# Performance work log

Hardware: AMD Instinct MI355X
Metric: run time of the kernel (lower is better)

## Reference

```python
import jax, jax.numpy as jnp
import numpy as np

NUM_NODES = 50000
D_IN = 256
D_OUT = 256
N_QUERIES = 128
PER_GROUP = 256            # edges per query group in the last step (> max_edges)
E1 = N_QUERIES * PER_GROUP # 32768
E0 = 32768
RATIO = 0.2                # ratio_update


def setup_inputs() -> dict:
    key = jax.random.key(0)
    ks = jax.random.split(key, 10)
    d4 = 4 * D_IN
    rng = np.random.default_rng(0)
    # last-step edges: col0 = query idx (sorted, equal-size groups), col6 = src, col7 = dst
    edges1 = np.zeros((E1, 8), np.int64)
    edges1[:, 0] = np.repeat(np.arange(N_QUERIES), PER_GROUP)
    edges1[:, 6] = rng.integers(0, NUM_NODES, E1)
    edges1[:, 7] = rng.integers(0, NUM_NODES, E1)
    # earlier-step edges
    edges0 = np.zeros((E0, 8), np.int64)
    edges0[:, 0] = rng.integers(0, N_QUERIES, E0)
    edges0[:, 6] = rng.integers(0, NUM_NODES, E0)
    edges0[:, 7] = rng.integers(0, NUM_NODES, E0)
    return {
        "visited_node_score": jax.random.uniform(ks[0], (NUM_NODES,), jnp.float32),
        "visited_node_representation": jax.random.normal(ks[1], (NUM_NODES, D_IN), jnp.float32),
        "selected_edges0": jnp.asarray(edges0),
        "selected_edges1": jnp.asarray(edges1),
        "rel_emb0": jax.random.normal(ks[2], (E0, D_IN), jnp.float32),
        "rel_emb1": jax.random.normal(ks[3], (E1, D_IN), jnp.float32),
        "query_src_ts_emb": jax.random.normal(ks[4], (N_QUERIES, D_IN), jnp.float32),
        "query_rel_emb": jax.random.normal(ks[5], (N_QUERIES, D_IN), jnp.float32),
        "Wq": jax.random.normal(ks[6], (d4, d4), jnp.float32) * np.sqrt(2.0 / d4),
        "Wk": jax.random.normal(ks[7], (d4, d4), jnp.float32) * np.sqrt(2.0 / d4),
        "Wl": jax.random.normal(ks[8], (D_OUT, D_IN), jnp.float32) * np.sqrt(2.0 / (D_IN + D_OUT)),
        "bl": jnp.zeros((D_OUT,), jnp.float32),
        "max_edges": 64,
    }


def _att_score(edges, node_repr, rel, qst_tab, qr_tab, Wq, Wk):
    # G3: sum(Q(cat(vi,rel,qst,qr)) * K(cat(vj,rel,qst,qr)), -1) per edge
    q, src, dst = edges[:, 0], edges[:, 6], edges[:, 7]
    qst, qr = qst_tab[q], qr_tab[q]
    left = jnp.concatenate([node_repr[src], rel, qst, qr], axis=-1)   # [E, 4d]
    right = jnp.concatenate([node_repr[dst], rel, qst, qr], axis=-1)  # [E, 4d]
    return jnp.sum((left @ Wq.T) * (right @ Wk.T), axis=-1)          # [E]


def _seg_softmax(logits, seg, n):
    m = jax.ops.segment_max(logits, seg, num_segments=n)
    e = jnp.exp(logits - m[seg])
    s = jax.ops.segment_sum(e, seg, num_segments=n)
    return e / s[seg]


def _update_repr(edges, node_repr, w, ratio):
    # sparse mm: out[src] += (1-ratio)*w_e*repr[dst]; + identity for non-src rows, + ratio*repr for src rows
    src, dst = edges[:, 6], edges[:, 7]
    n = node_repr.shape[0]
    agg = jax.ops.segment_sum(((1.0 - ratio) * w)[:, None] * node_repr[dst], src, num_segments=n)
    is_src = jnp.zeros((n,), bool).at[src].set(True)
    diag = jnp.where(is_src, ratio, 1.0)
    return agg + diag[:, None] * node_repr


def reference(visited_node_score, visited_node_representation, selected_edges0,
              selected_edges1, rel_emb0, rel_emb1, query_src_ts_emb, query_rel_emb,
              Wq, Wk, Wl, bl, max_edges):
    n = visited_node_representation.shape[0]
    nq = query_src_ts_emb.shape[0]
    pg = selected_edges1.shape[0] // nq
    # attention on last step's edges
    logits = _att_score(selected_edges1, visited_node_representation, rel_emb1,
                        query_src_ts_emb, query_rel_emb, Wq, Wk)
    src1 = selected_edges1[:, 6]
    src_score = visited_node_score[src1]
    soft = _seg_softmax(logits, src1, n)
    target = soft * src_score
    # per-query-group top-k pruning (each group has pg > k edges)
    _, ti = jax.lax.top_k(target.reshape(nq, pg), max_edges)  # [nq, k]
    orig_indices = (ti + (jnp.arange(nq) * pg)[:, None]).reshape(-1)
    pruned_edges = selected_edges1[orig_indices]
    pruned_src_score = src_score[orig_indices]
    pruned_soft = soft[orig_indices]
    # sparse scatter-aggregation of scores onto dst (col 7)
    updated_node_score = jax.ops.segment_sum(pruned_soft * pruned_src_score,
                                             pruned_edges[:, 7], num_segments=n)
    node_repr = _update_repr(pruned_edges, visited_node_representation, pruned_soft, RATIO)
    # back-propagate representations through the earlier step
    tl = _att_score(selected_edges0, node_repr, rel_emb0, query_src_ts_emb, query_rel_emb, Wq, Wk)
    ts = _seg_softmax(tl, selected_edges0[:, 6], n)
    node_repr = _update_repr(selected_edges0, node_repr, ts, RATIO)
    # bypass_forward: LeakyReLU(Linear(.))
    node_repr = jax.nn.leaky_relu(node_repr @ Wl.T + bl)
    return (updated_node_score, node_repr, pruned_edges, orig_indices)
```

## Files before the change

### kernel.cpp

```cpp
#include <hip/hip_runtime.h>

#define NN 50000
#define D 256
#define NQ 128
#define PG 256
#define NE 32768
#define ME 64
#define BCAP 32
#define KDIM 256
#define NKT 8

typedef _Float16 f16;
typedef __attribute__((ext_vector_type(4))) _Float16 f16x4;
typedef __attribute__((ext_vector_type(8))) _Float16 f16x8;
typedef __attribute__((ext_vector_type(4))) float f32x4;

#define MFMA16(a,b,c) __builtin_amdgcn_mfma_f32_16x16x32_f16(a,b,c,0,0,0)

__device__ __forceinline__ unsigned fenc(float f){
  unsigned b = __float_as_uint(f);
  return (b & 0x80000000u) ? ~b : (b | 0x80000000u);
}
__device__ __forceinline__ float fdec(unsigned u){
  unsigned b = (u & 0x80000000u) ? (u & 0x7fffffffu) : ~u;
  return __uint_as_float(b);
}
__device__ __forceinline__ void split8(float4 a, float4 b, f16x8& h, f16x8& l){
  float v[8] = {a.x,a.y,a.z,a.w,b.x,b.y,b.z,b.w};
#pragma unroll
  for (int i=0;i<8;++i){
    _Float16 hh = (_Float16)v[i];
    h[i] = hh;
    l[i] = (_Float16)(v[i] - (float)hh);
  }
}

template<int EPI>
__global__ __launch_bounds__(256) void hgemm(const float* __restrict__ A,
                                             int Mrows,
                                             const f16* __restrict__ Bh, const f16* __restrict__ Bl,
                                             float* __restrict__ C, int ldc,
                                             const float* __restrict__ bias)
{
  __shared__ f16 AsH[128*40], AsL[128*40], BsH[128*40], BsL[128*40];
  const int tid = threadIdx.x;
  const int rb = blockIdx.x*128, cb = blockIdx.y*128;
  const int row = tid >> 1, ko = (tid & 1)*16;
  const bool aok = (rb + row) < Mrows;
  const int lane = tid & 63, wv = tid >> 6;
  const int qrw = (wv & 1)*64, qcw = (wv >> 1)*64;
  const int lm = lane & 15, qd = lane >> 4;

  const float* gA = A + (size_t)(rb+row)*KDIM + ko;
  const f16* gBh = Bh + (size_t)(cb+row)*KDIM + ko;
  const f16* gBl = Bl + (size_t)(cb+row)*KDIM + ko;

  float4 pa0=make_float4(0.f,0.f,0.f,0.f), pa1=pa0, pa2=pa0, pa3=pa0;
  f16x8 pbh0, pbh1, pbl0, pbl1;
  if (aok){ pa0 = *(const float4*)gA;     pa1 = *(const float4*)(gA+4);
            pa2 = *(const float4*)(gA+8); pa3 = *(const float4*)(gA+12); }
  pbh0 = *(const f16x8*)gBh; pbh1 = *(const f16x8*)(gBh+8);
  pbl0 = *(const f16x8*)gBl; pbl1 = *(const f16x8*)(gBl+8);

  f32x4 acc[4][4];
#pragma unroll
  for (int t=0;t<4;++t)
#pragma unroll
    for (int u=0;u<4;++u)
#pragma unroll
      for (int r=0;r<4;++r) acc[t][u][r] = 0.f;

  const int wbase = row*40 + ko;
  for (int kt = 0; kt < NKT; ++kt){
    __syncthreads();
    {
      f16x8 h0,h1,l0,l1;
      split8(pa0,pa1,h0,l0); split8(pa2,pa3,h1,l1);
      *(f16x8*)(AsH + wbase) = h0; *(f16x8*)(AsH + wbase + 8) = h1;
      *(f16x8*)(AsL + wbase) = l0; *(f16x8*)(AsL + wbase + 8) = l1;
      *(f16x8*)(BsH + wbase) = pbh0; *(f16x8*)(BsH + wbase + 8) = pbh1;
      *(f16x8*)(BsL + wbase) = pbl0; *(f16x8*)(BsL + wbase + 8) = pbl1;
    }
    __syncthreads();
    if (kt+1 < NKT){
      const int k0 = (kt+1)*32;
      if (aok){ pa0 = *(const float4*)(gA + k0);     pa1 = *(const float4*)(gA + k0 + 4);
                pa2 = *(const float4*)(gA + k0 + 8); pa3 = *(const float4*)(gA + k0 + 12); }
      pbh0 = *(const f16x8*)(gBh + k0); pbh1 = *(const f16x8*)(gBh + k0 + 8);
      pbl0 = *(const f16x8*)(gBl + k0); pbl1 = *(const f16x8*)(gBl + k0 + 8);
    }
    f16x8 fah[4], fal[4], fbh[4], fbl[4];
#pragma unroll
    for (int t=0;t<4;++t){
      int off = (qrw + t*16 + lm)*40 + qd*8;
      fah[t] = *(const f16x8*)(AsH + off);
      fal[t] = *(const f16x8*)(AsL + off);
    }
#pragma unroll
    for (int u=0;u<4;++u){
      int off = (qcw + u*16 + lm)*40 + qd*8;
      fbh[u] = *(const f16x8*)(BsH + off);
      fbl[u] = *(const f16x8*)(BsL + off);
    }
#pragma unroll
    for (int t=0;t<4;++t)
#pragma unroll
      for (int u=0;u<4;++u){
        acc[t][u] = MFMA16(fah[t], fbh[u], acc[t][u]);
        acc[t][u] = MFMA16(fah[t], fbl[u], acc[t][u]);
        acc[t][u] = MFMA16(fal[t], fbh[u], acc[t][u]);
      }
  }
#pragma unroll
  for (int t=0;t<4;++t){
#pragma unroll
    for (int u=0;u<4;++u){
      int col = cb + qcw + u*16 + lm;
      f32x4 v = acc[t][u];
#pragma unroll
      for (int r=0;r<4;++r){
        int rg = rb + qrw + t*16 + qd*4 + r;
        if (rg < Mrows){
          float x = v[r];
          if (EPI==1){ x += bias[col]; x = x > 0.f ? x : 0.01f*x; }
          C[(size_t)rg*ldc + col] = x;
        }
      }
    }
  }
}

__global__ __launch_bounds__(256) void hgemm_rel(const float* __restrict__ A,
                                                 const f16* __restrict__ Bh, const f16* __restrict__ Bl,
                                                 const int* __restrict__ edges,
                                                 const float* __restrict__ H,
                                                 const float* __restrict__ Rel,
                                                 float* __restrict__ logits)
{
  __shared__ f16 AsH[128*40], AsL[128*40], BsH[128*40], BsL[128*40];
  __shared__ int sIdx[128];
  const int tid = threadIdx.x;
  const int rb = blockIdx.x*128, cb = blockIdx.y*128;
  const int sec = blockIdx.y >> 1;
  const int row = tid >> 1, ko = (tid & 1)*16;
  const int lane = tid & 63, wv = tid >> 6;
  const int qrw = (wv & 1)*64, qcw = (wv >> 1)*64;
  const int lm = lane & 15, qd = lane >> 4;

  if (tid < 128){
    int e = rb + tid;
    sIdx[tid] = (sec==0) ? edges[(size_t)e*8+6] : (sec==1 ? edges[(size_t)e*8+7] : 0);
  }

  const float* gA = A + (size_t)(rb+row)*KDIM + ko;
  const f16* gBh = Bh + (size_t)(cb+row)*KDIM + ko;
  const f16* gBl = Bl + (size_t)(cb+row)*KDIM + ko;

  float4 pa0 = *(const float4*)gA,     pa1 = *(const float4*)(gA+4);
  float4 pa2 = *(const float4*)(gA+8), pa3 = *(const float4*)(gA+12);
  f16x8 pbh0 = *(const f16x8*)gBh, pbh1 = *(const f16x8*)(gBh+8);
  f16x8 pbl0 = *(const f16x8*)gBl, pbl1 = *(const f16x8*)(gBl+8);

  f32x4 acc[4][4];
#pragma unroll
  for (int t=0;t<4;++t)
#pragma unroll
    for (int u=0;u<4;++u)
#pragma unroll
      for (int r=0;r<4;++r) acc[t][u][r] = 0.f;

  const int wbase = row*40 + ko;
  for (int kt = 0; kt < NKT; ++kt){
    __syncthreads();
    {
      f16x8 h0,h1,l0,l1;
      split8(pa0,pa1,h0,l0); split8(pa2,pa3,h1,l1);
      *(f16x8*)(AsH + wbase) = h0; *(f16x8*)(AsH + wbase + 8) = h1;
      *(f16x8*)(AsL + wbase) = l0; *(f16x8*)(AsL + wbase + 8) = l1;
      *(f16x8*)(BsH + wbase) = pbh0; *(f16x8*)(BsH + wbase + 8) = pbh1;
      *(f16x8*)(BsL + wbase) = pbl0; *(f16x8*)(BsL + wbase + 8) = pbl1;
    }
    __syncthreads();
    if (kt+1 < NKT){
      const int k0 = (kt+1)*32;
      pa0 = *(const float4*)(gA + k0);     pa1 = *(const float4*)(gA + k0 + 4);
      pa2 = *(const float4*)(gA + k0 + 8); pa3 = *(const float4*)(gA + k0 + 12);
      pbh0 = *(const f16x8*)(gBh + k0); pbh1 = *(const f16x8*)(gBh + k0 + 8);
      pbl0 = *(const f16x8*)(gBl + k0); pbl1 = *(const f16x8*)(gBl + k0 + 8);
    }
    f16x8 fah[4], fal[4], fbh[4], fbl[4];
#pragma unroll
    for (int t=0;t<4;++t){
      int off = (qrw + t*16 + lm)*40 + qd*8;
      fah[t] = *(const f16x8*)(AsH + off);
      fal[t] = *(const f16x8*)(AsL + off);
    }
#pragma unroll
    for (int u=0;u<4;++u){
      int off = (qcw + u*16 + lm)*40 + qd*8;
      fbh[u] = *(const f16x8*)(BsH + off);
      fbl[u] = *(const f16x8*)(BsL + off);
    }
#pragma unroll
    for (int t=0;t<4;++t)
#pragma unroll
      for (int u=0;u<4;++u){
        acc[t][u] = MFMA16(fah[t], fbh[u], acc[t][u]);
        acc[t][u] = MFMA16(fah[t], fbl[u], acc[t][u]);
        acc[t][u] = MFMA16(fal[t], fbh[u], acc[t][u]);
      }
  }
  const int cbase = ((blockIdx.y & 1)*128) + qcw + lm;
#pragma unroll
  for (int t=0;t<4;++t){
#pragma unroll
    for (int r=0;r<4;++r){
      int lrow = qrw + t*16 + qd*4 + r;
      int e = rb + lrow;
      const float* xb = (sec==2) ? (Rel + (size_t)e*256)
                                 : (H + (size_t)sIdx[lrow]*256);
      float p = acc[t][0][r]*xb[cbase]
              + acc[t][1][r]*xb[cbase+16]
              + acc[t][2][r]*xb[cbase+32]
              + acc[t][3][r]*xb[cbase+48];
      p += __shfl_xor(p, 1); p += __shfl_xor(p, 2);
      p += __shfl_xor(p, 4); p += __shfl_xor(p, 8);
      if (lm == 0) atomicAdd(logits + e, p);
    }
  }
}

__global__ void split_f16(const float* __restrict__ X, f16* __restrict__ Xh,
                          f16* __restrict__ Xl, int n)
{
  int i = (blockIdx.x*256 + threadIdx.x)*4;
  if (i >= n) return;
  float4 v = *(const float4*)(X+i);
  f16x4 h, l;
  h[0]=(_Float16)v.x; h[1]=(_Float16)v.y; h[2]=(_Float16)v.z; h[3]=(_Float16)v.w;
  l[0]=(_Float16)(v.x-(float)h[0]); l[1]=(_Float16)(v.y-(float)h[1]);
  l[2]=(_Float16)(v.z-(float)h[2]); l[3]=(_Float16)(v.w-(float)h[3]);
  *(f16x4*)(Xh+i)=h; *(f16x4*)(Xl+i)=l;
}

__global__ void build_bt_mhh(const float* __restrict__ M, f16* __restrict__ Bh, f16* __restrict__ Bl)
{
  int idx = blockIdx.x*256 + threadIdx.x;
  int n = idx >> 8, k = idx & 255;
  float v = M[(size_t)k*1024 + n];
  _Float16 h = (_Float16)v;
  Bh[idx] = h; Bl[idx] = (_Float16)(v - (float)h);
}

__global__ void build_bt_wcat(const float* __restrict__ M, f16* __restrict__ Bh, f16* __restrict__ Bl)
{
  int idx = blockIdx.x*256 + threadIdx.x;
  int j = idx >> 8, k = idx & 255;
  float v;
  if (j < 256)      v = M[(size_t)j*1024 + 256 + k];
  else if (j < 512) v = M[(size_t)(256+k)*1024 + (j-256)];
  else              v = M[(size_t)(256 + j-512)*1024 + 256 + k];
  _Float16 h = (_Float16)v;
  Bh[idx] = h; Bl[idx] = (_Float16)(v - (float)h);
}

__global__ __launch_bounds__(256) void gemm_tn_split(const float* __restrict__ A,
                                                     const float* __restrict__ B,
                                                     double* __restrict__ Cpart)
{
  __shared__ __align__(16) double As[16*98];
  __shared__ __align__(16) double Bs[16*98];
  const int tid = threadIdx.x;
  const int rb = blockIdx.x * 64, cb = blockIdx.y * 64;
  const int z  = blockIdx.z;
  const int ty = tid >> 4, tx = tid & 15;
  const int aj = tid >> 4, ag = tid & 15;
  double acc[4][4] = {};
  const int jbeg = z * 128;

  const float* gA = A + (size_t)(jbeg+aj)*1024 + rb + ag*4;
  const float* gB = B + (size_t)(jbeg+aj)*1024 + cb + ag*4;
  float4 av = *(const float4*)gA;
  float4 bv = *(const float4*)gB;

  const int wbase = aj*98 + ag*6;
  const int aoff  = ty*6, boff = tx*6;

  for (int t0 = 0; t0 < 8; ++t0) {
    __syncthreads();
    {
      double2* wa = (double2*)(As + wbase);
      double2* wb = (double2*)(Bs + wbase);
      wa[0] = make_double2((double)av.x, (double)av.y);
      wa[1] = make_double2((double)av.z, (double)av.w);
      wb[0] = make_double2((double)bv.x, (double)bv.y);
      wb[1] = make_double2((double)bv.z, (double)bv.w);
    }
    __syncthreads();
    if (t0 < 7){
      gA += 16*1024; gB += 16*1024;
      av = *(const float4*)gA;
      bv = *(const float4*)gB;
    }
#pragma unroll
    for (int jj=0; jj<16; ++jj){
      const double* pa = As + jj*98 + aoff;
      const double* pb = Bs + jj*98 + boff;
      double2 a01 = *(const double2*)(pa);
      double2 a23 = *(const double2*)(pa+2);
      double2 b01 = *(const double2*)(pb);
      double2 b23 = *(const double2*)(pb+2);
      double a0=a01.x, a1=a01.y, a2=a23.x, a3=a23.y;
      double b0=b01.x, b1=b01.y, b2=b23.x, b3=b23.y;
      acc[0][0]+=a0*b0; acc[0][1]+=a0*b1; acc[0][2]+=a0*b2; acc[0][3]+=a0*b3;
      acc[1][0]+=a1*b0; acc[1][1]+=a1*b1; acc[1][2]+=a1*b2; acc[1][3]+=a1*b3;
      acc[2][0]+=a2*b0; acc[2][1]+=a2*b1; acc[2][2]+=a2*b2; acc[2][3]+=a2*b3;
      acc[3][0]+=a3*b0; acc[3][1]+=a3*b1; acc[3][2]+=a3*b2; acc[3][3]+=a3*b3;
    }
  }
  double* Cz = Cpart + (size_t)z * 1048576;
#pragma unroll
  for (int i=0;i<4;++i)
#pragma unroll
    for (int j=0;j<4;++j)
      Cz[(size_t)(rb+ty*4+i)*1024 + cb+tx*4+j] = acc[i][j];
}

__global__ void reduce_m(const double* __restrict__ P, float* __restrict__ Mout)
{
  int i = blockIdx.x*256 + threadIdx.x;
  double s = 0.0;
#pragma unroll
  for (int z=0;z<8;++z) s += P[(size_t)i + (size_t)z*1048576];
  Mout[i] = (float)s;
}

__global__ void build_g(const float* __restrict__ qst, const float* __restrict__ qr,
                        float* __restrict__ G)
{
  int idx = blockIdx.x*256 + threadIdx.x;
  int q = idx >> 9, k = idx & 511;
  G[idx] = (k < 256) ? qst[(size_t)q*256 + k] : qr[(size_t)q*256 + k - 256];
}

__global__ void build_bq(const float* __restrict__ M, float* __restrict__ Bq)
{
  int idx = blockIdx.x*256 + threadIdx.x;
  int k = idx / 1280, t = idx - k*1280;
  float v;
  if (t < 256)      v = M[(size_t)t*1024 + 512 + k];
  else if (t < 512) v = M[(size_t)(512+k)*1024 + (t-256)];
  else if (t < 768) v = M[(size_t)(256+(t-512))*1024 + 512 + k]
                      + M[(size_t)(512+k)*1024 + 256 + (t-512)];
  else              v = M[(size_t)(512+k)*1024 + 512 + (t-768)];
  Bq[idx] = v;
}

__global__ __launch_bounds__(256) void gemm64(const float* __restrict__ A, int lda,
                                              const float* __restrict__ B, int ldb,
                                              float* __restrict__ C, int ldc,
                                              int Mrows, int Kdim)
{
  __shared__ float As[16][68];
  __shared__ float Bs[16][68];
  const int tid = threadIdx.x;
  const int rb = blockIdx.x*64, cb = blockIdx.y*64;
  const int tx = tid & 15, ty = tid >> 4;
  const int a_r = tid >> 2, a_k = (tid & 3)*4;
  const int b_c = tid & 63, b_r0 = (tid >> 6)*4;
  const bool aok = (rb + a_r) < Mrows;
  float4 pa = make_float4(0.f,0.f,0.f,0.f);
  float pb[4];
  if (aok) pa = *(const float4*)(A + (size_t)(rb+a_r)*lda + a_k);
#pragma unroll
  for (int j=0;j<4;++j) pb[j] = B[(size_t)(b_r0+j)*ldb + cb + b_c];
  float acc[4][4] = {};
  const int NK = Kdim >> 4;
  for (int t0=0; t0<NK; ++t0){
    __syncthreads();
    As[a_k+0][a_r]=pa.x; As[a_k+1][a_r]=pa.y; As[a_k+2][a_r]=pa.z; As[a_k+3][a_r]=pa.w;
#pragma unroll
    for (int j=0;j<4;++j) Bs[b_r0+j][b_c] = pb[j];
    __syncthreads();
    if (t0+1 < NK){
      int k0 = (t0+1) << 4;
      if (aok) pa = *(const float4*)(A + (size_t)(rb+a_r)*lda + k0 + a_k);
#pragma unroll
      for (int j=0;j<4;++j) pb[j] = B[(size_t)(k0+b_r0+j)*ldb + cb + b_c];
    }
#pragma unroll
    for (int kk=0;kk<16;++kk){
      float a[4], b[4];
      *(float4*)&a[0] = *(const float4*)&As[kk][ty*4];
#pragma unroll
      for (int j=0;j<4;++j) b[j] = Bs[kk][tx + 16*j];
#pragma unroll
      for (int i=0;i<4;++i)
#pragma unroll
        for (int j=0;j<4;++j) acc[i][j] += a[i]*b[j];
    }
  }
#pragma unroll
  for (int i=0;i<4;++i){
    int r = rb + ty*4 + i;
    if (r < Mrows)
#pragma unroll
      for (int j=0;j<4;++j)
        C[(size_t)r*ldc + cb + tx + 16*j] = acc[i][j];
  }
}

__global__ __launch_bounds__(256) void qc_dot(const float* __restrict__ Ccat,
    const float* __restrict__ qst, const float* __restrict__ qr, float* __restrict__ qc)
{
  __shared__ float red[256];
  int q = blockIdx.x, t = threadIdx.x;
  float a = Ccat[(size_t)q*1280 + 768 + t]  * qst[(size_t)q*256 + t]
          + Ccat[(size_t)q*1280 + 1024 + t] * qr [(size_t)q*256 + t];
  red[t] = a;
  __syncthreads();
  for (int s=128; s>0; s>>=1){
    if (t < s) red[t] += red[t+s];
    __syncthreads();
  }
  if (t==0) qc[q] = red[0];
}

__global__ __launch_bounds__(256) void slim_logits(const int* __restrict__ edges,
    const float* __restrict__ H, const float* __restrict__ U,
    const float* __restrict__ Rel,
    const float* __restrict__ Ct, const float* __restrict__ qc,
    float* __restrict__ logits)
{
  int lane = threadIdx.x & 63;
  int e = blockIdx.x*4 + (threadIdx.x >> 6);
  int q   = edges[(size_t)e*8 + 0];
  int src = edges[(size_t)e*8 + 6];
  int dst = edges[(size_t)e*8 + 7];
  const float4* hs = (const float4*)(H   + (size_t)src*256);
  const float4* hd = (const float4*)(H   + (size_t)dst*256);
  const float4* us = (const float4*)(U   + (size_t)src*256);
  const float4* rl = (const float4*)(Rel + (size_t)e*256);
  const float4* t1 = (const float4*)(Ct + (size_t)q*1280);
  const float4* t2 = (const float4*)(Ct + (size_t)q*1280 + 256);
  const float4* w4 = (const float4*)(Ct + (size_t)q*1280 + 512);
  float4 a, b, c;
  float s = 0.f;
  a = hd[lane]; b = us[lane]; c = t2[lane];
  s += a.x*(b.x+c.x) + a.y*(b.y+c.y) + a.z*(b.z+c.z) + a.w*(b.w+c.w);
  a = hs[lane]; c = t1[lane];
  s += a.x*c.x + a.y*c.y + a.z*c.z + a.w*c.w;
  a = rl[lane]; c = w4[lane];
  s += a.x*c.x + a.y*c.y + a.z*c.z + a.w*c.w;
#pragma unroll
  for (int off=32; off>0; off>>=1) s += __shfl_down(s, off);
  if (lane==0) logits[e] = s + qc[q];
}

__global__ void segmax_k(const int* __restrict__ edges, const float* __restrict__ logits,
                         unsigned* __restrict__ menc, int nE)
{
  int e = blockIdx.x*256 + threadIdx.x; if (e >= nE) return;
  atomicMax(menc + edges[(size_t)e*8+6], fenc(logits[e]));
}
__global__ void segexp_k(const int* __restrict__ edges, const float* __restrict__ logits,
                         const unsigned* __restrict__ menc, float* __restrict__ ebuf,
                         float* __restrict__ ssum, int nE)
{
  int e = blockIdx.x*256 + threadIdx.x; if (e >= nE) return;
  int s = edges[(size_t)e*8+6];
  float ex = expf(logits[e] - fdec(menc[s]));
  ebuf[e] = ex;
  atomicAdd(ssum + s, ex);
}
template<int TGT>
__global__ void segsoft_k(const int* __restrict__ edges, const float* __restrict__ ebuf,
                          const float* __restrict__ ssum, float* __restrict__ soft,
                          const float* __restrict__ score, float* __restrict__ target, int nE)
{
  int e = blockIdx.x*256 + threadIdx.x; if (e >= nE) return;
  int s = edges[(size_t)e*8+6];
  float so = ebuf[e] / ssum[s];
  soft[e] = so;
  if (TGT) target[e] = so * score[s];
}

__global__ __launch_bounds__(256) void topk_k(const float* __restrict__ target,
    const float* __restrict__ soft, const int* __restrict__ edges1,
    float* __restrict__ out0, float* __restrict__ out2, float* __restrict__ out3,
    int* __restrict__ p_src, int* __restrict__ p_dst, float* __restrict__ p_w)
{
  int qb = blockIdx.x, t = threadIdx.x;
  __shared__ float v[256];
  __shared__ int   ix[256];
  v[t] = target[(size_t)qb*256 + t];
  ix[t] = t;
  __syncthreads();
  for (int k=2; k<=256; k<<=1){
    for (int j=k>>1; j>0; j>>=1){
      int ixj = t ^ j;
      if (ixj > t){
        float va=v[t], vb=v[ixj]; int ia=ix[t], ib=ix[ixj];
        bool dir  = ((t & k) == 0);
        bool l_ab = (va > vb) || (va == vb && ia < ib);
        bool sw   = dir ? (!l_ab) : l_ab;
        if (sw){ v[t]=vb; v[ixj]=va; ix[t]=ib; ix[ixj]=ia; }
      }
      __syncthreads();
    }
  }
  if (t < 64){
    int oi = qb*256 + ix[t];
    int o  = qb*64 + t;
    out3[o] = (float)oi;
#pragma unroll
    for (int c2=0;c2<8;++c2) out2[(size_t)o*8 + c2] = (float)edges1[(size_t)oi*8 + c2];
    int s_ = edges1[(size_t)oi*8+6], d_ = edges1[(size_t)oi*8+7];
    p_src[o] = s_; p_dst[o] = d_; p_w[o] = soft[oi];
    atomicAdd(out0 + d_, v[t]);
  }
}

__global__ void bucket_fill(const int* __restrict__ srcarr, int stride, int n,
                            int* __restrict__ counts, int* __restrict__ bucket,
                            int* __restrict__ over, int* __restrict__ n_over)
{
  int e = blockIdx.x*256 + threadIdx.x; if (e >= n) return;
  int s = srcarr[(size_t)e*stride];
  int pos = atomicAdd(counts + s, 1);
  if (pos < BCAP) bucket[(size_t)s*BCAP + pos] = e;
  else { int oi = atomicAdd(n_over, 1); over[oi] = e; }
}

__global__ __launch_bounds__(256) void fused_update(const int* __restrict__ counts,
    const int* __restrict__ bucket, const int* __restrict__ dstarr, int dstride,
    const float* __restrict__ w, const float* __restrict__ Hin, float* __restrict__ Hout)
{
  int lane = threadIdx.x & 63;
  int n = blockIdx.x*4 + (threadIdx.x >> 6);
  if (n >= NN) return;
  int cnt = counts[n];
  float fac = cnt > 0 ? 0.2f : 1.0f;
  float4 h = ((const float4*)(Hin + (size_t)n*256))[lane];
  float4 acc = make_float4(fac*h.x, fac*h.y, fac*h.z, fac*h.w);
  int m = cnt < BCAP ? cnt : BCAP;
  for (int i=0;i<m;++i){
    int e = bucket[(size_t)n*BCAP + i];
    int d = dstarr[(size_t)e*dstride];
    float f = 0.8f * w[e];
    float4 vv = ((const float4*)(Hin + (size_t)d*256))[lane];
    acc.x += f*vv.x; acc.y += f*vv.y; acc.z += f*vv.z; acc.w += f*vv.w;
  }
  ((float4*)(Hout + (size_t)n*256))[lane] = acc;
}

__global__ __launch_bounds__(256) void over_k(const int* __restrict__ over,
    const int* __restrict__ n_over,
    const int* __restrict__ srcarr, int sstride,
    const int* __restrict__ dstarr, int dstride,
    const float* __restrict__ w, const float* __restrict__ Hin, float* __restrict__ Hout)
{
  int lane = threadIdx.x & 63;
  int i = blockIdx.x*4 + (threadIdx.x >> 6);
  if (i >= *n_over) return;
  int e = over[i];
  int s = srcarr[(size_t)e*sstride], d = dstarr[(size_t)e*dstride];
  float f = 0.8f * w[e];
  float4 vv = ((const float4*)(Hin + (size_t)d*256))[lane];
  float* o = Hout + (size_t)s*256 + lane*4;
  atomicAdd(o+0, f*vv.x); atomicAdd(o+1, f*vv.y);
  atomicAdd(o+2, f*vv.z); atomicAdd(o+3, f*vv.w);
}

extern "C" void kernel_launch(void* const* d_in, const int* in_sizes, int n_in,
                              void* d_out, int out_size, void* d_ws, size_t ws_size,
                              hipStream_t stream)
{
  const float* score = (const float*)d_in[0];
  const float* H0    = (const float*)d_in[1];
  const int*   edges0= (const int*)d_in[2];
  const int*   edges1= (const int*)d_in[3];
  const float* rel0  = (const float*)d_in[4];
  const float* rel1  = (const float*)d_in[5];
  const float* qst   = (const float*)d_in[6];
  const float* qr    = (const float*)d_in[7];
  const float* Wq    = (const float*)d_in[8];
  const float* Wk    = (const float*)d_in[9];
  const float* Wl    = (const float*)d_in[10];
  const float* bl    = (const float*)d_in[11];
  (void)in_sizes; (void)n_in; (void)out_size; (void)ws_size;

  float* out0 = (float*)d_out;
  float* out1 = out0 + NN;
  float* out2 = out1 + (size_t)NN*D;
  float* out3 = out2 + (size_t)NQ*ME*8;

  float* ws     = (float*)d_ws;
  float* Mbuf   = ws;
  float* Ccat   = ws + 1048576;
  float* qcv    = ws + 1212416;
  float* G      = ws + 1212544;
  float* logits = ws + 1278080;
  float* ebuf   = ws + 1310848;
  float* soft   = ws + 1343616;
  float* target = ws + 1376384;
  unsigned* menc= (unsigned*)(ws + 1409152);
  float* ssum   = ws + 1459152;
  int* p_src    = (int*)(ws + 1509152);
  int* p_dst    = (int*)(ws + 1517344);
  float* p_w    = ws + 1525536;
  float* Bq     = ws + 1533728;
  float* U      = ws + 2189088;
  float* Hnew   = ws + 14989088;
  float* SCR    = ws + 27789088;
  int* counts = (int*)SCR;
  int* n_over = (int*)(SCR + 50000);
  int* over   = (int*)(SCR + 50056);
  int* bucket = (int*)(SCR + 100000);
  float* P0   = SCR + 2000000;
  double* Mpart = (double*)P0;
  f16* mhh_h  = (f16*)P0;
  f16* mhh_l  = (f16*)(P0 + 32768);
  f16* wcat_h = (f16*)(P0 + 65536);
  f16* wcat_l = (f16*)(P0 + 163840);
  f16* wl_h   = (f16*)(P0 + 262144);
  f16* wl_l   = (f16*)(P0 + 294912);
  float* Hpre = U;

  hipMemsetAsync(out0, 0, (size_t)NN*4, stream);
  hipMemsetAsync(menc, 0, (size_t)NN*4, stream);
  hipMemsetAsync(ssum, 0, (size_t)NN*4, stream);

  gemm_tn_split<<<dim3(16,16,8), 256, 0, stream>>>(Wq, Wk, Mpart);
  reduce_m<<<4096, 256, 0, stream>>>(Mpart, Mbuf);
  build_g<<<256, 256, 0, stream>>>(qst, qr, G);
  build_bq<<<2560, 256, 0, stream>>>(Mbuf, Bq);
  gemm64<<<dim3(2,20), 256, 0, stream>>>(G, 512, Bq, 1280, Ccat, 1280, NQ, 512);
  qc_dot<<<NQ, 256, 0, stream>>>(Ccat, qst, qr, qcv);
  build_bt_mhh<<<256, 256, 0, stream>>>(Mbuf, mhh_h, mhh_l);
  build_bt_wcat<<<768, 256, 0, stream>>>(Mbuf, wcat_h, wcat_l);
  split_f16<<<64, 256, 0, stream>>>(Wl, wl_h, wl_l, 65536);

  hgemm<0><<<dim3(391,2), 256, 0, stream>>>(H0, NN, mhh_h, mhh_l, U, 256, nullptr);
  slim_logits<<<NE/4, 256, 0, stream>>>(edges1, H0, U, rel1, Ccat, qcv, logits);
  hgemm_rel<<<dim3(256,6), 256, 0, stream>>>(rel1, wcat_h, wcat_l, edges1, H0, rel1, logits);

  segmax_k<<<NE/256, 256, 0, stream>>>(edges1, logits, menc, NE);
  segexp_k<<<NE/256, 256, 0, stream>>>(edges1, logits, menc, ebuf, ssum, NE);
  segsoft_k<1><<<NE/256, 256, 0, stream>>>(edges1, ebuf, ssum, soft, score, target, NE);

  topk_k<<<NQ, 256, 0, stream>>>(target, soft, edges1, out0, out2, out3, p_src, p_dst, p_w);

  hipMemsetAsync(counts, 0, (size_t)NN*4, stream);
  hipMemsetAsync(n_over, 0, 4, stream);
  bucket_fill<<<(NQ*ME+255)/256, 256, 0, stream>>>(p_src, 1, NQ*ME, counts, bucket, over, n_over);
  fused_update<<<(NN+3)/4, 256, 0, stream>>>(counts, bucket, p_dst, 1, p_w, H0, Hnew);
  over_k<<<(NQ*ME)/4, 256, 0, stream>>>(over, n_over, p_src, 1, p_dst, 1, p_w, H0, Hnew);

  hipMemsetAsync(menc, 0, (size_t)NN*4, stream);
  hipMemsetAsync(ssum, 0, (size_t)NN*4, stream);

  hgemm<0><<<dim3(391,2), 256, 0, stream>>>(Hnew, NN, mhh_h, mhh_l, U, 256, nullptr);
  slim_logits<<<NE/4, 256, 0, stream>>>(edges0, Hnew, U, rel0, Ccat, qcv, logits);
  hgemm_rel<<<dim3(256,6), 256, 0, stream>>>(rel0, wcat_h, wcat_l, edges0, Hnew, rel0, logits);

  segmax_k<<<NE/256, 256, 0, stream>>>(edges0, logits, menc, NE);
  segexp_k<<<NE/256, 256, 0, stream>>>(edges0, logits, menc, ebuf, ssum, NE);
  segsoft_k<0><<<NE/256, 256, 0, stream>>>(edges0, ebuf, ssum, soft, nullptr, nullptr, NE);

  hipMemsetAsync(counts, 0, (size_t)NN*4, stream);
  hipMemsetAsync(n_over, 0, 4, stream);
  bucket_fill<<<NE/256, 256, 0, stream>>>(edges0 + 6, 8, NE, counts, bucket, over, n_over);
  fused_update<<<(NN+3)/4, 256, 0, stream>>>(counts, bucket, edges0 + 7, 8, soft, Hnew, Hpre);
  over_k<<<NE/4, 256, 0, stream>>>(over, n_over, edges0 + 6, 8, edges0 + 7, 8, soft, Hnew, Hpre);

  hgemm<1><<<dim3(391,2), 256, 0, stream>>>(Hpre, NN, wl_h, wl_l, out1, 256, bl);
}
```

Baseline: 618.9 us.

## Widen hgemm tiles to full 256 columns with 512-thread blocks

The split-fp16 GEMM kernels now use 512-thread blocks that each compute a 128x256 output tile instead of two 128x128 tiles. Each A row block is loaded from global memory and split into high/low halves only once rather than once per column half. This cuts redundant A traffic and conversion work, at the cost of larger shared memory and fewer, bigger blocks, which may lower occupancy.

```diff
diff --git a/kernel.cpp b/kernel.cpp
--- a/kernel.cpp
+++ b/kernel.cpp
@@ -36,29 +36,29 @@
 }
 
 template<int EPI>
-__global__ __launch_bounds__(256) void hgemm(const float* __restrict__ A,
+__global__ __launch_bounds__(512) void hgemm(const float* __restrict__ A,
                                              int Mrows,
                                              const f16* __restrict__ Bh, const f16* __restrict__ Bl,
                                              float* __restrict__ C, int ldc,
                                              const float* __restrict__ bias)
 {
-  __shared__ f16 AsH[128*40], AsL[128*40], BsH[128*40], BsL[128*40];
+  __shared__ f16 AsH[128*40], AsL[128*40], BsH[256*40], BsL[256*40];
   const int tid = threadIdx.x;
-  const int rb = blockIdx.x*128, cb = blockIdx.y*128;
-  const int row = tid >> 1, ko = (tid & 1)*16;
-  const bool aok = (rb + row) < Mrows;
+  const int rb = blockIdx.x*128;
+  const int arow = tid >> 2, ako = (tid & 3)*8;
+  const int brow = tid >> 1, bko = (tid & 1)*16;
+  const bool aok = (rb + arow) < Mrows;
   const int lane = tid & 63, wv = tid >> 6;
   const int qrw = (wv & 1)*64, qcw = (wv >> 1)*64;
   const int lm = lane & 15, qd = lane >> 4;
 
-  const float* gA = A + (size_t)(rb+row)*KDIM + ko;
-  const f16* gBh = Bh + (size_t)(cb+row)*KDIM + ko;
-  const f16* gBl = Bl + (size_t)(cb+row)*KDIM + ko;
-
-  float4 pa0=make_float4(0.f,0.f,0.f,0.f), pa1=pa0, pa2=pa0, pa3=pa0;
+  const float* gA = A + (size_t)(rb+arow)*KDIM + ako;
+  const f16* gBh = Bh + (size_t)brow*KDIM + bko;
+  const f16* gBl = Bl + (size_t)brow*KDIM + bko;
+
+  float4 pa0=make_float4(0.f,0.f,0.f,0.f), pa1=pa0;
   f16x8 pbh0, pbh1, pbl0, pbl1;
-  if (aok){ pa0 = *(const float4*)gA;     pa1 = *(const float4*)(gA+4);
-            pa2 = *(const float4*)(gA+8); pa3 = *(const float4*)(gA+12); }
+  if (aok){ pa0 = *(const float4*)gA; pa1 = *(const float4*)(gA+4); }
   pbh0 = *(const f16x8*)gBh; pbh1 = *(const f16x8*)(gBh+8);
   pbl0 = *(const f16x8*)gBl; pbl1 = *(const f16x8*)(gBl+8);
 
@@ -70,22 +70,22 @@
 #pragma unroll
       for (int r=0;r<4;++r) acc[t][u][r] = 0.f;
 
-  const int wbase = row*40 + ko;
+  const int wabase = arow*40 + ako;
+  const int wbbase = brow*40 + bko;
   for (int kt = 0; kt < NKT; ++kt){
     __syncthreads();
     {
-      f16x8 h0,h1,l0,l1;
-      split8(pa0,pa1,h0,l0); split8(pa2,pa3,h1,l1);
-      *(f16x8*)(AsH + wbase) = h0; *(f16x8*)(AsH + wbase + 8) = h1;
-      *(f16x8*)(AsL + wbase) = l0; *(f16x8*)(AsL + wbase + 8) = l1;
-      *(f16x8*)(BsH + wbase) = pbh0; *(f16x8*)(BsH + wbase + 8) = pbh1;
-      *(f16x8*)(BsL + wbase) = pbl0; *(f16x8*)(BsL + wbase + 8) = pbl1;
+      f16x8 h0,l0;
+      split8(pa0,pa1,h0,l0);
+      *(f16x8*)(AsH + wabase) = h0;
+      *(f16x8*)(AsL + wabase) = l0;
+      *(f16x8*)(BsH + wbbase) = pbh0; *(f16x8*)(BsH + wbbase + 8) = pbh1;
+      *(f16x8*)(BsL + wbbase) = pbl0; *(f16x8*)(BsL + wbbase + 8) = pbl1;
     }
     __syncthreads();
     if (kt+1 < NKT){
       const int k0 = (kt+1)*32;
-      if (aok){ pa0 = *(const float4*)(gA + k0);     pa1 = *(const float4*)(gA + k0 + 4);
-                pa2 = *(const float4*)(gA + k0 + 8); pa3 = *(const float4*)(gA + k0 + 12); }
+      if (aok){ pa0 = *(const float4*)(gA + k0); pa1 = *(const float4*)(gA + k0 + 4); }
       pbh0 = *(const f16x8*)(gBh + k0); pbh1 = *(const f16x8*)(gBh + k0 + 8);
       pbl0 = *(const f16x8*)(gBl + k0); pbl1 = *(const f16x8*)(gBl + k0 + 8);
     }
@@ -115,7 +115,7 @@
   for (int t=0;t<4;++t){
 #pragma unroll
     for (int u=0;u<4;++u){
-      int col = cb + qcw + u*16 + lm;
+      int col = qcw + u*16 + lm;
       f32x4 v = acc[t][u];
 #pragma unroll
       for (int r=0;r<4;++r){
@@ -130,19 +130,21 @@
   }
 }
 
-__global__ __launch_bounds__(256) void hgemm_rel(const float* __restrict__ A,
+__global__ __launch_bounds__(512) void hgemm_rel(const float* __restrict__ A,
                                                  const f16* __restrict__ Bh, const f16* __restrict__ Bl,
                                                  const int* __restrict__ edges,
                                                  const float* __restrict__ H,
                                                  const float* __restrict__ Rel,
                                                  float* __restrict__ logits)
 {
-  __shared__ f16 AsH[128*40], AsL[128*40], BsH[128*40], BsL[128*40];
+  __shared__ f16 AsH[128*40], AsL[128*40], BsH[256*40], BsL[256*40];
   __shared__ int sIdx[128];
   const int tid = threadIdx.x;
-  const int rb = blockIdx.x*128, cb = blockIdx.y*128;
-  const int sec = blockIdx.y >> 1;
-  const int row = tid >> 1, ko = (tid & 1)*16;
+  const int rb = blockIdx.x*128;
+  const int sec = blockIdx.y;
+  const int cb = sec*256;
+  const int arow = tid >> 2, ako = (tid & 3)*8;
+  const int brow = tid >> 1, bko = (tid & 1)*16;
   const int lane = tid & 63, wv = tid >> 6;
   const int qrw = (wv & 1)*64, qcw = (wv >> 1)*64;
   const int lm = lane & 15, qd = lane >> 4;
@@ -152,12 +154,11 @@
     sIdx[tid] = (sec==0) ? edges[(size_t)e*8+6] : (sec==1 ? edges[(size_t)e*8+7] : 0);
   }
 
-  const float* gA = A + (size_t)(rb+row)*KDIM + ko;
-  const f16* gBh = Bh + (size_t)(cb+row)*KDIM + ko;
-  const f16* gBl = Bl + (size_t)(cb+row)*KDIM + ko;
-
-  float4 pa0 = *(const float4*)gA,     pa1 = *(const float4*)(gA+4);
-  float4 pa2 = *(const float4*)(gA+8), pa3 = *(const float4*)(gA+12);
+  const float* gA = A + (size_t)(rb+arow)*KDIM + ako;
+  const f16* gBh = Bh + (size_t)(cb+brow)*KDIM + bko;
+  const f16* gBl = Bl + (size_t)(cb+brow)*KDIM + bko;
+
+  float4 pa0 = *(const float4*)gA, pa1 = *(const float4*)(gA+4);
   f16x8 pbh0 = *(const f16x8*)gBh, pbh1 = *(const f16x8*)(gBh+8);
   f16x8 pbl0 = *(const f16x8*)gBl, pbl1 = *(const f16x8*)(gBl+8);
 
@@ -169,22 +170,22 @@
 #pragma unroll
       for (int r=0;r<4;++r) acc[t][u][r] = 0.f;
 
-  const int wbase = row*40 + ko;
+  const int wabase = arow*40 + ako;
+  const int wbbase = brow*40 + bko;
   for (int kt = 0; kt < NKT; ++kt){
     __syncthreads();
     {
-      f16x8 h0,h1,l0,l1;
-      split8(pa0,pa1,h0,l0); split8(pa2,pa3,h1,l1);
-      *(f16x8*)(AsH + wbase) = h0; *(f16x8*)(AsH + wbase + 8) = h1;
-      *(f16x8*)(AsL + wbase) = l0; *(f16x8*)(AsL + wbase + 8) = l1;
-      *(f16x8*)(BsH + wbase) = pbh0; *(f16x8*)(BsH + wbase + 8) = pbh1;
-      *(f16x8*)(BsL + wbase) = pbl0; *(f16x8*)(BsL + wbase + 8) = pbl1;
+      f16x8 h0,l0;
+      split8(pa0,pa1,h0,l0);
+      *(f16x8*)(AsH + wabase) = h0;
+      *(f16x8*)(AsL + wabase) = l0;
+      *(f16x8*)(BsH + wbbase) = pbh0; *(f16x8*)(BsH + wbbase + 8) = pbh1;
+      *(f16x8*)(BsL + wbbase) = pbl0; *(f16x8*)(BsL + wbbase + 8) = pbl1;
     }
     __syncthreads();
     if (kt+1 < NKT){
       const int k0 = (kt+1)*32;
-      pa0 = *(const float4*)(gA + k0);     pa1 = *(const float4*)(gA + k0 + 4);
-      pa2 = *(const float4*)(gA + k0 + 8); pa3 = *(const float4*)(gA + k0 + 12);
+      pa0 = *(const float4*)(gA + k0); pa1 = *(const float4*)(gA + k0 + 4);
       pbh0 = *(const f16x8*)(gBh + k0); pbh1 = *(const f16x8*)(gBh + k0 + 8);
       pbl0 = *(const f16x8*)(gBl + k0); pbl1 = *(const f16x8*)(gBl + k0 + 8);
     }
@@ -210,7 +211,7 @@
         acc[t][u] = MFMA16(fal[t], fbh[u], acc[t][u]);
       }
   }
-  const int cbase = ((blockIdx.y & 1)*128) + qcw + lm;
+  const int cbase = qcw + lm;
 #pragma unroll
   for (int t=0;t<4;++t){
 #pragma unroll
@@ -641,9 +642,9 @@
   build_bt_wcat<<<768, 256, 0, stream>>>(Mbuf, wcat_h, wcat_l);
   split_f16<<<64, 256, 0, stream>>>(Wl, wl_h, wl_l, 65536);
 
-  hgemm<0><<<dim3(391,2), 256, 0, stream>>>(H0, NN, mhh_h, mhh_l, U, 256, nullptr);
+  hgemm<0><<<dim3(391), 512, 0, stream>>>(H0, NN, mhh_h, mhh_l, U, 256, nullptr);
   slim_logits<<<NE/4, 256, 0, stream>>>(edges1, H0, U, rel1, Ccat, qcv, logits);
-  hgemm_rel<<<dim3(256,6), 256, 0, stream>>>(rel1, wcat_h, wcat_l, edges1, H0, rel1, logits);
+  hgemm_rel<<<dim3(256,3), 512, 0, stream>>>(rel1, wcat_h, wcat_l, edges1, H0, rel1, logits);
 
   segmax_k<<<NE/256, 256, 0, stream>>>(edges1, logits, menc, NE);
   segexp_k<<<NE/256, 256, 0, stream>>>(edges1, logits, menc, ebuf, ssum, NE);
@@ -660,9 +661,9 @@
   hipMemsetAsync(menc, 0, (size_t)NN*4, stream);
   hipMemsetAsync(ssum, 0, (size_t)NN*4, stream);
 
-  hgemm<0><<<dim3(391,2), 256, 0, stream>>>(Hnew, NN, mhh_h, mhh_l, U, 256, nullptr);
+  hgemm<0><<<dim3(391), 512, 0, stream>>>(Hnew, NN, mhh_h, mhh_l, U, 256, nullptr);
   slim_logits<<<NE/4, 256, 0, stream>>>(edges0, Hnew, U, rel0, Ccat, qcv, logits);
-  hgemm_rel<<<dim3(256,6), 256, 0, stream>>>(rel0, wcat_h, wcat_l, edges0, Hnew, rel0, logits);
+  hgemm_rel<<<dim3(256,3), 512, 0, stream>>>(rel0, wcat_h, wcat_l, edges0, Hnew, rel0, logits);
 
   segmax_k<<<NE/256, 256, 0, stream>>>(edges0, logits, menc, NE);
   segexp_k<<<NE/256, 256, 0, stream>>>(edges0, logits, menc, ebuf, ssum, NE);
@@ -674,5 +675,5 @@
   fused_update<<<(NN+3)/4, 256, 0, stream>>>(counts, bucket, edges0 + 7, 8, soft, Hnew, Hpre);
   over_k<<<NE/4, 256, 0, stream>>>(over, n_over, edges0 + 6, 8, edges0 + 7, 8, soft, Hnew, Hpre);
 
-  hgemm<1><<<dim3(391,2), 256, 0, stream>>>(Hpre, NN, wl_h, wl_l, out1, 256, bl);
-}
+  hgemm<1><<<dim3(391), 512, 0, stream>>>(Hpre, NN, wl_h, wl_l, out1, 256, bl);
+}
```

Result: faster. 600.4 us (-3.0%).
